# Kernel tuning notes

Hardware: AMD Instinct MI355X
Metric: run time of the kernel (lower is better)

## Reference

```python
import jax, jax.numpy as jnp
import numpy as np

N_NODES, N_EDGES, D_IN, D_HID, D_OUT = 50000, 800000, 128, 64, 32


def _glorot(key, shape):
    lim = jnp.sqrt(6.0 / (shape[0] + shape[1]))
    return jax.random.uniform(key, shape, minval=-lim, maxval=lim, dtype=jnp.float32)


def setup_inputs() -> dict:
    key = jax.random.key(0)
    ks = jax.random.split(key, 12)
    return {
        "x": jax.random.normal(ks[0], (N_NODES, D_IN), jnp.float32),
        "edge_index": jax.random.randint(ks[1], (2, N_EDGES), 0, N_NODES, dtype=jnp.int64),
        "edge_weight": jax.random.uniform(ks[2], (N_EDGES,), jnp.float32),
        # layer 1: GATv2Conv(D_IN -> D_HID, heads=1, edge_dim=1)
        "Wl1": _glorot(ks[3], (D_HID, D_IN)), "bl1": jnp.zeros((D_HID,), jnp.float32),
        "Wr1": _glorot(ks[4], (D_HID, D_IN)), "br1": jnp.zeros((D_HID,), jnp.float32),
        "We1": _glorot(ks[5], (D_HID, 1)),
        "att1": _glorot(ks[6], (1, D_HID))[0],
        "bias1": jnp.zeros((D_HID,), jnp.float32),
        # layer 2: GATv2Conv(D_HID -> D_OUT, heads=1, edge_dim=1)
        "Wl2": _glorot(ks[7], (D_OUT, D_HID)), "bl2": jnp.zeros((D_OUT,), jnp.float32),
        "Wr2": _glorot(ks[8], (D_OUT, D_HID)), "br2": jnp.zeros((D_OUT,), jnp.float32),
        "We2": _glorot(ks[9], (D_OUT, 1)),
        "att2": _glorot(ks[10], (1, D_OUT))[0],
        "bias2": jnp.zeros((D_OUT,), jnp.float32),
    }


def _segment_softmax(scores, seg, n):
    m = jax.ops.segment_max(scores, seg, num_segments=n)
    e = jnp.exp(scores - m[seg])
    s = jax.ops.segment_sum(e, seg, num_segments=n)
    return e / s[seg]


def _gatv2(x, src, dst, attr, Wl, bl, Wr, br, We, att, bias, n):
    # PyG GATv2Conv, heads=1, share_weights=False
    xl = x @ Wl.T + bl                    # source transform  [N, D]
    xr = x @ Wr.T + br                    # target transform  [N, D]
    ea = attr @ We.T                      # edge-attr embed   [E, D]
    m = jax.nn.leaky_relu(xl[src] + xr[dst] + ea, negative_slope=0.2)
    score = m @ att                       # [E]
    alpha = _segment_softmax(score, dst, n)
    out = jax.ops.segment_sum(alpha[:, None] * xl[src], dst, num_segments=n)
    return out + bias


def _forward(x, edge_index, edge_weight,
             Wl1, bl1, Wr1, br1, We1, att1, bias1,
             Wl2, bl2, Wr2, br2, We2, att2, bias2):
    n = x.shape[0]
    src, dst = edge_index[0], edge_index[1]
    attr = edge_weight[:, None]           # edge_dim = 1
    # PyG add_self_loops (default True) with fill_value='mean':
    # self-loop attr = mean of incoming edge_attr per node (0 if none)
    cnt = jax.ops.segment_sum(jnp.ones_like(edge_weight), dst, num_segments=n)
    loop_attr = jax.ops.segment_sum(attr, dst, num_segments=n) / jnp.maximum(cnt, 1.0)[:, None]
    loop = jnp.arange(n, dtype=src.dtype)
    src2 = jnp.concatenate([src, loop])
    dst2 = jnp.concatenate([dst, loop])
    attr2 = jnp.concatenate([attr, loop_attr], axis=0)
    h = jax.nn.elu(_gatv2(x, src2, dst2, attr2, Wl1, bl1, Wr1, br1, We1, att1, bias1, n))
    z = _gatv2(h, src2, dst2, attr2, Wl2, bl2, Wr2, br2, We2, att2, bias2, n)
    return jax.nn.softplus(z) + 0.0001


def reference(x, edge_index, edge_weight,
              Wl1, bl1, Wr1, br1, We1, att1, bias1,
              Wl2, bl2, Wr2, br2, We2, att2, bias2):
    return _forward(x, edge_index, edge_weight,
                    Wl1, bl1, Wr1, br1, We1, att1, bias1,
                    Wl2, bl2, Wr2, br2, We2, att2, bias2)
```

## Files before the change

kernel.cpp:

```cpp
#include <hip/hip_runtime.h>
#include <math.h>

typedef unsigned short ushort_t;
typedef __attribute__((ext_vector_type(8))) short bf16x8;
typedef __attribute__((ext_vector_type(4))) float f32x4;

#define NBLK  128
#define MAXNH 25024

template<int CTRL>
__device__ __forceinline__ float dpp_addf(float x)
{
    int y = __builtin_amdgcn_update_dpp(0, __float_as_int(x), CTRL, 0xf, 0xf, true);
    return x + __int_as_float(y);
}

template<int LPE>
__device__ __forceinline__ float group_reduce(float p)
{
    p = dpp_addf<0xB1>(p);
    p = dpp_addf<0x4E>(p);
    if constexpr (LPE >= 8)  p = dpp_addf<0x141>(p);
    if constexpr (LPE >= 16) p = dpp_addf<0x140>(p);
    return p;
}

__device__ __forceinline__ ushort_t f2bf(float f)
{
    unsigned u = __float_as_uint(f);
    return (ushort_t)((u + 0x7fffu + ((u >> 16) & 1u)) >> 16);
}

__global__ __launch_bounds__(256)
void setup_kernel(const float* __restrict__ Wl1, const float* __restrict__ Wr1,
                  const float* __restrict__ Wl2, const float* __restrict__ Wr2,
                  ushort_t* __restrict__ wab1, ushort_t* __restrict__ wab2)
{
    const int T = gridDim.x * 256;
    const int i0 = blockIdx.x * 256 + threadIdx.x;
    for (int k = i0; k < 2 * 64 * 128; k += T)
        wab1[k] = f2bf(k < 64 * 128 ? Wl1[k] : Wr1[k - 64 * 128]);
    for (int k = i0; k < 2 * 32 * 64; k += T)
        wab2[k] = f2bf(k < 32 * 64 ? Wl2[k] : Wr2[k - 32 * 64]);
}

__global__ __launch_bounds__(256, 1)
void count_hist(const int* __restrict__ ei, ushort_t* __restrict__ lrank,
                ushort_t* __restrict__ histG, int E, int n, int EPB)
{
    __shared__ unsigned h[MAXNH];
    const int tid = threadIdx.x;
    const int b   = blockIdx.x;
    const int nh  = (n + 1) >> 1;
    for (int i = tid; i < nh; i += 256) h[i] = 0u;
    __syncthreads();

    const int e0 = b * EPB;
    const int e1 = min(e0 + EPB, E);
    for (int e = e0 + tid; e < e1; e += 256) {
        int d = ei[E + e];
        unsigned sh  = (unsigned)(d & 1) * 16u;
        unsigned old = atomicAdd(&h[d >> 1], 1u << sh);
        lrank[e] = (ushort_t)((old >> sh) & 0xffffu);
    }
    __syncthreads();

    ushort_t* row = histG + (size_t)b * n;
    for (int i = tid; i < n; i += 256) {
        unsigned v = h[i >> 1];
        row[i] = (ushort_t)((v >> ((i & 1) * 16)) & 0xffffu);
    }
}

__global__ __launch_bounds__(256)
void col_scan(ushort_t* __restrict__ histG, int* __restrict__ cnt, int n)
{
    int idx = blockIdx.x * 256 + threadIdx.x;
    if (idx >= n) return;
    unsigned acc = 0;
    #pragma unroll 1
    for (int b0 = 0; b0 < NBLK; b0 += 16) {
        ushort_t c[16];
        #pragma unroll
        for (int j = 0; j < 16; ++j)
            c[j] = histG[(size_t)(b0 + j) * n + idx];
        #pragma unroll
        for (int j = 0; j < 16; ++j) {
            unsigned cc = c[j];
            histG[(size_t)(b0 + j) * n + idx] = (ushort_t)acc;
            acc += cc;
        }
    }
    cnt[idx] = (int)acc;
}

__global__ __launch_bounds__(256)
void scan_p1(const int* __restrict__ cnt, int* __restrict__ bsums, int n)
{
    __shared__ int s[256];
    const int tid = threadIdx.x;
    int gi = blockIdx.x * 256 + tid;
    s[tid] = (gi < n) ? cnt[gi] : 0;
    __syncthreads();
    #pragma unroll
    for (int off = 128; off >= 1; off >>= 1) {
        if (tid < off) s[tid] += s[tid + off];
        __syncthreads();
    }
    if (tid == 0) bsums[blockIdx.x] = s[0];
}

__global__ __launch_bounds__(256)
void scan_p3(const int* __restrict__ cnt, const int* __restrict__ bsums,
             int* __restrict__ row_off, int n, int nb)
{
    __shared__ int sb[256];
    __shared__ int s[256];
    const int tid = threadIdx.x;

    int bv = (tid < nb) ? bsums[tid] : 0;
    sb[tid] = bv;
    __syncthreads();
    #pragma unroll
    for (int off = 1; off < 256; off <<= 1) {
        int t = (tid >= off) ? sb[tid - off] : 0;
        __syncthreads();
        sb[tid] += t;
        __syncthreads();
    }
    int excl_t = sb[tid] - bv;
    __syncthreads();
    sb[tid] = excl_t;
    __syncthreads();
    const int base = sb[blockIdx.x];

    int gi = blockIdx.x * 256 + tid;
    int c = (gi < n) ? cnt[gi] : 0;
    s[tid] = c;
    __syncthreads();
    #pragma unroll
    for (int off = 1; off < 256; off <<= 1) {
        int t = (tid >= off) ? s[tid - off] : 0;
        __syncthreads();
        s[tid] += t;
        __syncthreads();
    }
    if (gi < n) {
        int excl = base + s[tid] - c;
        row_off[gi] = excl;
        if (gi == n - 1) row_off[n] = excl + c;
    }
}

template<int N, int K>
__global__ __launch_bounds__(256, 2)
void scat_plus_gemm(const int* __restrict__ ei, const float* __restrict__ ew,
                    const int* __restrict__ row_off,
                    const ushort_t* __restrict__ lrank,
                    const ushort_t* __restrict__ boff,
                    int2* __restrict__ slot,
                    int E, int n, int EPB, int scatBlocks,
                    const float* __restrict__ X, const ushort_t* __restrict__ Wab,
                    const float* __restrict__ ba, const float* __restrict__ bb,
                    ushort_t* __restrict__ OutA, ushort_t* __restrict__ OutB, int M)
{
    constexpr int KC = K / 32;
    constexpr int NT = N / 16;
    __shared__ ushort_t sW[N * K];
    __shared__ ushort_t sX[64 * K];
    const int tid = threadIdx.x;

    if (blockIdx.x < scatBlocks) {
        const int base = blockIdx.x * (256 * 8);
        #pragma unroll
        for (int k = 0; k < 8; ++k) {
            int e = base + k * 256 + tid;
            if (e < E) {
                int d  = ei[E + e];
                int hb = e / EPB;
                int pos = row_off[d] + (int)boff[(size_t)hb * n + d]
                                     + (int)lrank[e];
                slot[pos] = make_int2(ei[e], __float_as_int(ew[e]));
            }
        }
        return;
    }

    const int m0 = (blockIdx.x - scatBlocks) * 64;

    auto swz = [](int r, int e) {
        return r * K + ((((e >> 3) ^ (r & 7)) << 3) | (e & 7));
    };

    constexpr int WQ8 = N * K / 8;
    for (int q = tid; q < WQ8; q += 256) {
        int nrow = q / (K / 8);
        int e8   = (q % (K / 8)) * 8;
        uint4 v = *(const uint4*)(Wab + (size_t)nrow * K + e8);
        *(uint4*)&sW[swz(nrow, e8)] = v;
    }
    constexpr int XQ = 64 * (K / 4);
    for (int q = tid; q < XQ; q += 256) {
        int r  = q / (K / 4);
        int k4 = (q % (K / 4)) * 4;
        float4 v = make_float4(0.f, 0.f, 0.f, 0.f);
        int gr = m0 + r;
        if (gr < M) v = *(const float4*)(X + (size_t)gr * K + k4);
        short4 h = make_short4((short)f2bf(v.x), (short)f2bf(v.y),
                               (short)f2bf(v.z), (short)f2bf(v.w));
        *(short4*)&sX[swz(r, k4)] = h;
    }
    __syncthreads();

    const int wv   = tid >> 6;
    const int lane = tid & 63;
    const int mrow = lane & 15;
    const int quad = lane >> 4;

    bf16x8 a[KC];
    #pragma unroll
    for (int kc = 0; kc < KC; ++kc)
        a[kc] = *(const bf16x8*)&sX[swz(wv * 16 + mrow, kc * 32 + quad * 8)];

    #pragma unroll
    for (int nt = 0; nt < NT; ++nt) {
        f32x4 acc = {0.f, 0.f, 0.f, 0.f};
        #pragma unroll
        for (int kc = 0; kc < KC; ++kc) {
            bf16x8 bfr = *(const bf16x8*)&sW[swz(nt * 16 + mrow, kc * 32 + quad * 8)];
            acc = __builtin_amdgcn_mfma_f32_16x16x32_bf16(a[kc], bfr, acc, 0, 0, 0);
        }
        const int col = nt * 16 + mrow;
        ushort_t* dst;
        int cc;
        float bv;
        if (col < N / 2) { dst = OutA; cc = col;         bv = ba[cc]; }
        else             { dst = OutB; cc = col - N / 2; bv = bb[cc]; }
        #pragma unroll
        for (int r = 0; r < 4; ++r) {
            int row = m0 + wv * 16 + quad * 4 + r;
            if (row < M)
                dst[(size_t)row * (N / 2) + cc] = f2bf(acc[r] + bv);
        }
    }
}

template<int N, int K>
__global__ __launch_bounds__(256, 2)
void gemm_xw_mfma(const float* __restrict__ X, const ushort_t* __restrict__ Wab,
                  const float* __restrict__ ba, const float* __restrict__ bb,
                  ushort_t* __restrict__ OutA, ushort_t* __restrict__ OutB, int M)
{
    constexpr int KC = K / 32;
    constexpr int NT = N / 16;
    __shared__ ushort_t sW[N * K];
    __shared__ ushort_t sX[64 * K];
    const int tid = threadIdx.x;
    const int m0  = blockIdx.x * 64;

    auto swz = [](int r, int e) {
        return r * K + ((((e >> 3) ^ (r & 7)) << 3) | (e & 7));
    };

    constexpr int WQ8 = N * K / 8;
    for (int q = tid; q < WQ8; q += 256) {
        int nrow = q / (K / 8);
        int e8   = (q % (K / 8)) * 8;
        uint4 v = *(const uint4*)(Wab + (size_t)nrow * K + e8);
        *(uint4*)&sW[swz(nrow, e8)] = v;
    }
    constexpr int XQ = 64 * (K / 4);
    for (int q = tid; q < XQ; q += 256) {
        int r  = q / (K / 4);
        int k4 = (q % (K / 4)) * 4;
        float4 v = make_float4(0.f, 0.f, 0.f, 0.f);
        int gr = m0 + r;
        if (gr < M) v = *(const float4*)(X + (size_t)gr * K + k4);
        short4 h = make_short4((short)f2bf(v.x), (short)f2bf(v.y),
                               (short)f2bf(v.z), (short)f2bf(v.w));
        *(short4*)&sX[swz(r, k4)] = h;
    }
    __syncthreads();

    const int wv   = tid >> 6;
    const int lane = tid & 63;
    const int mrow = lane & 15;
    const int quad = lane >> 4;

    bf16x8 a[KC];
    #pragma unroll
    for (int kc = 0; kc < KC; ++kc)
        a[kc] = *(const bf16x8*)&sX[swz(wv * 16 + mrow, kc * 32 + quad * 8)];

    #pragma unroll
    for (int nt = 0; nt < NT; ++nt) {
        f32x4 acc = {0.f, 0.f, 0.f, 0.f};
        #pragma unroll
        for (int kc = 0; kc < KC; ++kc) {
            bf16x8 bfr = *(const bf16x8*)&sW[swz(nt * 16 + mrow, kc * 32 + quad * 8)];
            acc = __builtin_amdgcn_mfma_f32_16x16x32_bf16(a[kc], bfr, acc, 0, 0, 0);
        }
        const int col = nt * 16 + mrow;
        ushort_t* dst;
        int cc;
        float bv;
        if (col < N / 2) { dst = OutA; cc = col;         bv = ba[cc]; }
        else             { dst = OutB; cc = col - N / 2; bv = bb[cc]; }
        #pragma unroll
        for (int r = 0; r < 4; ++r) {
            int row = m0 + wv * 16 + quad * 4 + r;
            if (row < M)
                dst[(size_t)row * (N / 2) + cc] = f2bf(acc[r] + bv);
        }
    }
}

template<int D, int ACT>
__global__ __launch_bounds__(256)
void edge_attn(const ushort_t* __restrict__ xl, const ushort_t* __restrict__ xr,
               const float* __restrict__ We, const float* __restrict__ att,
               const float* __restrict__ bias,
               const int* __restrict__ row_off, const int2* __restrict__ slot,
               float* __restrict__ out, int n)
{
    constexpr int LPE = D / 4;
    constexpr int SG  = 64 / LPE;
    const int lane = threadIdx.x & 63;
    const int wid  = threadIdx.x >> 6;
    const int t    = lane % LPE;
    const int g    = lane / LPE;
    const int node = blockIdx.x * 4 + wid;
    if (node >= n) return;

    auto unpack = [](uint2 d) -> float4 {
        float4 r;
        r.x = __uint_as_float(d.x << 16);
        r.y = __uint_as_float(d.x & 0xffff0000u);
        r.z = __uint_as_float(d.y << 16);
        r.w = __uint_as_float(d.y & 0xffff0000u);
        return r;
    };

    const float4 We4   = *(const float4*)(We   + 4 * t);
    const float4 att4  = *(const float4*)(att  + 4 * t);
    const float4 bias4 = *(const float4*)(bias + 4 * t);
    const float4 xr4   = unpack(*(const uint2*)(xr + (size_t)node * D + 4 * t));

    const int start = row_off[node];
    const int end   = row_off[node + 1];
    const int R  = (end - start) / SG;
    const int jt = start + R * SG;
    const bool has_tail = jt < end;

    int2  q[4];
    uint2 xv[4];
    #pragma unroll
    for (int s = 0; s < 4; ++s) {
        if (s < R) {
            q[s]  = slot[start + s * SG + g];
            xv[s] = *(const uint2*)(xl + (size_t)q[s].x * D + 4 * t);
        }
    }
    int2 tq = make_int2(0, 0);
    uint2 tx = make_uint2(0u, 0u);
    if (has_tail) {
        int idx = min(jt + g, end - 1);
        tq = slot[idx];
        tx = *(const uint2*)(xl + (size_t)tq.x * D + 4 * t);
    }
    const uint2 xs = *(const uint2*)(xl + (size_t)node * D + 4 * t);

    float denom = 0.f, wsum = 0.f;
    float4 acc = make_float4(0.f, 0.f, 0.f, 0.f);

    auto body = [&](int2 qe, float4 xvv, bool active) {
        float w = __int_as_float(qe.y);
        float4 v;
        v.x = xvv.x + fmaf(w, We4.x, xr4.x);
        v.y = xvv.y + fmaf(w, We4.y, xr4.y);
        v.z = xvv.z + fmaf(w, We4.z, xr4.z);
        v.w = xvv.w + fmaf(w, We4.w, xr4.w);
        float4 m;
        m.x = fmaxf(v.x, 0.2f * v.x);
        m.y = fmaxf(v.y, 0.2f * v.y);
        m.z = fmaxf(v.z, 0.2f * v.z);
        m.w = fmaxf(v.w, 0.2f * v.w);
        float p = att4.x * m.x + att4.y * m.y + att4.z * m.z + att4.w * m.w;
        p = group_reduce<LPE>(p);
        float e = active ? __expf(p) : 0.f;
        wsum  += active ? w : 0.f;
        denom += e;
        acc.x = fmaf(e, xvv.x, acc.x);
        acc.y = fmaf(e, xvv.y, acc.y);
        acc.z = fmaf(e, xvv.z, acc.z);
        acc.w = fmaf(e, xvv.w, acc.w);
    };

    int b = 0;
    for (; b + 4 <= R; b += 4) {
        #pragma unroll
        for (int s = 0; s < 4; ++s) {
            int2 cq = q[s]; uint2 cx = xv[s];
            int nr = b + 4 + s;
            if (nr < R) {
                q[s]  = slot[start + nr * SG + g];
                xv[s] = *(const uint2*)(xl + (size_t)q[s].x * D + 4 * t);
            }
            body(cq, unpack(cx), true);
        }
    }
    #pragma unroll
    for (int s = 0; s < 4; ++s)
        if (b + s < R) body(q[s], unpack(xv[s]), true);

    if (has_tail)
        body(tq, unpack(tx), (jt + g) < end);

    #pragma unroll
    for (int mask = LPE; mask < 64; mask <<= 1) {
        denom += __shfl_xor(denom, mask);
        wsum  += __shfl_xor(wsum,  mask);
        acc.x += __shfl_xor(acc.x, mask);
        acc.y += __shfl_xor(acc.y, mask);
        acc.z += __shfl_xor(acc.z, mask);
        acc.w += __shfl_xor(acc.w, mask);
    }

    {
        float w = wsum / (float)max(end - start, 1);
        float4 xvs = unpack(xs);
        float4 v;
        v.x = xvs.x + fmaf(w, We4.x, xr4.x);
        v.y = xvs.y + fmaf(w, We4.y, xr4.y);
        v.z = xvs.z + fmaf(w, We4.z, xr4.z);
        v.w = xvs.w + fmaf(w, We4.w, xr4.w);
        float4 m;
        m.x = fmaxf(v.x, 0.2f * v.x);
        m.y = fmaxf(v.y, 0.2f * v.y);
        m.z = fmaxf(v.z, 0.2f * v.z);
        m.w = fmaxf(v.w, 0.2f * v.w);
        float p = att4.x * m.x + att4.y * m.y + att4.z * m.z + att4.w * m.w;
        p = group_reduce<LPE>(p);
        float e = __expf(p);
        denom += e;
        acc.x = fmaf(e, xvs.x, acc.x);
        acc.y = fmaf(e, xvs.y, acc.y);
        acc.z = fmaf(e, xvs.z, acc.z);
        acc.w = fmaf(e, xvs.w, acc.w);
    }

    float4 res;
    res.x = acc.x / denom + bias4.x;
    res.y = acc.y / denom + bias4.y;
    res.z = acc.z / denom + bias4.z;
    res.w = acc.w / denom + bias4.w;
    if (ACT == 0) {
        res.x = fmaxf(res.x, 0.f) + __expf(fminf(res.x, 0.f)) - 1.f;
        res.y = fmaxf(res.y, 0.f) + __expf(fminf(res.y, 0.f)) - 1.f;
        res.z = fmaxf(res.z, 0.f) + __expf(fminf(res.z, 0.f)) - 1.f;
        res.w = fmaxf(res.w, 0.f) + __expf(fminf(res.w, 0.f)) - 1.f;
    } else {
        res.x = fmaxf(res.x, 0.f) + __logf(1.f + __expf(-fabsf(res.x))) + 1e-4f;
        res.y = fmaxf(res.y, 0.f) + __logf(1.f + __expf(-fabsf(res.y))) + 1e-4f;
        res.z = fmaxf(res.z, 0.f) + __logf(1.f + __expf(-fabsf(res.z))) + 1e-4f;
        res.w = fmaxf(res.w, 0.f) + __logf(1.f + __expf(-fabsf(res.w))) + 1e-4f;
    }
    if (g == 0)
        *(float4*)(out + (size_t)node * D + 4 * t) = res;
}

extern "C" void kernel_launch(void* const* d_in, const int* in_sizes, int n_in,
                              void* d_out, int out_size, void* d_ws, size_t ws_size,
                              hipStream_t stream)
{
    const float* x     = (const float*)d_in[0];
    const int*   ei    = (const int*)d_in[1];
    const float* ew    = (const float*)d_in[2];
    const float* Wl1   = (const float*)d_in[3];
    const float* bl1   = (const float*)d_in[4];
    const float* Wr1   = (const float*)d_in[5];
    const float* br1   = (const float*)d_in[6];
    const float* We1   = (const float*)d_in[7];
    const float* att1  = (const float*)d_in[8];
    const float* bias1 = (const float*)d_in[9];
    const float* Wl2   = (const float*)d_in[10];
    const float* bl2   = (const float*)d_in[11];
    const float* Wr2   = (const float*)d_in[12];
    const float* br2   = (const float*)d_in[13];
    const float* We2   = (const float*)d_in[14];
    const float* att2  = (const float*)d_in[15];
    const float* bias2 = (const float*)d_in[16];
    float* out = (float*)d_out;

    const int n = in_sizes[0] / 128;
    const int E = in_sizes[2];
    const int NB = (n + 255) / 256;
    const int EPB = (E + NBLK - 1) / NBLK;
    const int scatBlocks = (E + 2047) / 2048;
    const int gemmBlocks = (n + 63) / 64;

    char* wp = (char*)d_ws;
    auto carve = [&](size_t bytes) -> void* {
        void* p = (void*)wp;
        wp += (bytes + 255) & ~(size_t)255;
        return p;
    };
    int*      cnt     = (int*)     carve((size_t)n * 4);
    int*      row_off = (int*)     carve((size_t)(n + 1) * 4);
    ushort_t* lrank   = (ushort_t*)carve((size_t)E * 2);
    ushort_t* histG   = (ushort_t*)carve((size_t)NBLK * n * 2);
    int*      bsums   = (int*)     carve((size_t)256 * 4);
    int2*     slot    = (int2*)    carve((size_t)E * 8);
    ushort_t* wab1    = (ushort_t*)carve((size_t)2 * 64 * 128 * 2);
    ushort_t* wab2    = (ushort_t*)carve((size_t)2 * 32 * 64 * 2);
    ushort_t* xl1     = (ushort_t*)carve((size_t)n * 64 * 2);
    ushort_t* xr1     = (ushort_t*)carve((size_t)n * 64 * 2);
    float*    hbuf    = (float*)   carve((size_t)n * 64 * 4);
    ushort_t* xl2     = (ushort_t*)carve((size_t)n * 32 * 2);
    ushort_t* xr2     = (ushort_t*)carve((size_t)n * 32 * 2);

    setup_kernel<<<256, 256, 0, stream>>>(Wl1, Wr1, Wl2, Wr2, wab1, wab2);

    count_hist<<<NBLK, 256, 0, stream>>>(ei, lrank, histG, E, n, EPB);
    col_scan  <<<NB, 256, 0, stream>>>(histG, cnt, n);
    scan_p1   <<<NB, 256, 0, stream>>>(cnt, bsums, n);
    scan_p3   <<<NB, 256, 0, stream>>>(cnt, bsums, row_off, n, NB);

    scat_plus_gemm<128, 128><<<scatBlocks + gemmBlocks, 256, 0, stream>>>(
        ei, ew, row_off, lrank, histG, slot, E, n, EPB, scatBlocks,
        x, wab1, bl1, br1, xl1, xr1, n);

    edge_attn<64, 0><<<(n + 3) / 4, 256, 0, stream>>>(xl1, xr1, We1, att1, bias1,
                                                      row_off, slot, hbuf, n);
    gemm_xw_mfma<64, 64><<<(n + 63) / 64, 256, 0, stream>>>(hbuf, wab2, bl2, br2,
                                                            xl2, xr2, n);
    edge_attn<32, 1><<<(n + 3) / 4, 256, 0, stream>>>(xl2, xr2, We2, att2, bias2,
                                                      row_off, slot, out, n);
}
```

Before: 244.0 us.

## Fold setup into histogram, fuse column scan with GEMM, scatter via LDS offsets

Weight bf16 conversion moves into an extra block of the histogram kernel. The column scan and block-sum reduction now run in the same launch as the layer-1 GEMM. The edge scatter becomes its own kernel with one block per histogram chunk, loading that block's offset row into LDS so the random global reads of per-block offsets disappear. This cuts the launch count and overlaps the scan with the GEMM, but the scatter now runs with only 128 blocks instead of being spread across the GEMM launch.

```diff
diff --git a/kernel.cpp b/kernel.cpp
--- a/kernel.cpp
+++ b/kernel.cpp
@@ -31,27 +31,27 @@
     return (ushort_t)((u + 0x7fffu + ((u >> 16) & 1u)) >> 16);
 }
 
-__global__ __launch_bounds__(256)
-void setup_kernel(const float* __restrict__ Wl1, const float* __restrict__ Wr1,
-                  const float* __restrict__ Wl2, const float* __restrict__ Wr2,
-                  ushort_t* __restrict__ wab1, ushort_t* __restrict__ wab2)
-{
-    const int T = gridDim.x * 256;
-    const int i0 = blockIdx.x * 256 + threadIdx.x;
-    for (int k = i0; k < 2 * 64 * 128; k += T)
-        wab1[k] = f2bf(k < 64 * 128 ? Wl1[k] : Wr1[k - 64 * 128]);
-    for (int k = i0; k < 2 * 32 * 64; k += T)
-        wab2[k] = f2bf(k < 32 * 64 ? Wl2[k] : Wr2[k - 32 * 64]);
-}
-
 __global__ __launch_bounds__(256, 1)
 void count_hist(const int* __restrict__ ei, ushort_t* __restrict__ lrank,
-                ushort_t* __restrict__ histG, int E, int n, int EPB)
-{
-    __shared__ unsigned h[MAXNH];
+                ushort_t* __restrict__ histG,
+                const float* __restrict__ Wl1, const float* __restrict__ Wr1,
+                const float* __restrict__ Wl2, const float* __restrict__ Wr2,
+                ushort_t* __restrict__ wab1, ushort_t* __restrict__ wab2,
+                int E, int n, int EPB)
+{
     const int tid = threadIdx.x;
     const int b   = blockIdx.x;
-    const int nh  = (n + 1) >> 1;
+
+    if (b == NBLK) {
+        for (int k = tid; k < 2 * 64 * 128; k += 256)
+            wab1[k] = f2bf(k < 64 * 128 ? Wl1[k] : Wr1[k - 64 * 128]);
+        for (int k = tid; k < 2 * 32 * 64; k += 256)
+            wab2[k] = f2bf(k < 32 * 64 ? Wl2[k] : Wr2[k - 32 * 64]);
+        return;
+    }
+
+    __shared__ unsigned h[MAXNH];
+    const int nh = (n + 1) >> 1;
     for (int i = tid; i < nh; i += 256) h[i] = 0u;
     __syncthreads();
 
@@ -72,121 +72,53 @@
     }
 }
 
-__global__ __launch_bounds__(256)
-void col_scan(ushort_t* __restrict__ histG, int* __restrict__ cnt, int n)
-{
-    int idx = blockIdx.x * 256 + threadIdx.x;
-    if (idx >= n) return;
-    unsigned acc = 0;
-    #pragma unroll 1
-    for (int b0 = 0; b0 < NBLK; b0 += 16) {
-        ushort_t c[16];
-        #pragma unroll
-        for (int j = 0; j < 16; ++j)
-            c[j] = histG[(size_t)(b0 + j) * n + idx];
-        #pragma unroll
-        for (int j = 0; j < 16; ++j) {
-            unsigned cc = c[j];
-            histG[(size_t)(b0 + j) * n + idx] = (ushort_t)acc;
-            acc += cc;
-        }
-    }
-    cnt[idx] = (int)acc;
-}
-
-__global__ __launch_bounds__(256)
-void scan_p1(const int* __restrict__ cnt, int* __restrict__ bsums, int n)
-{
-    __shared__ int s[256];
-    const int tid = threadIdx.x;
-    int gi = blockIdx.x * 256 + tid;
-    s[tid] = (gi < n) ? cnt[gi] : 0;
-    __syncthreads();
-    #pragma unroll
-    for (int off = 128; off >= 1; off >>= 1) {
-        if (tid < off) s[tid] += s[tid + off];
-        __syncthreads();
-    }
-    if (tid == 0) bsums[blockIdx.x] = s[0];
-}
-
-__global__ __launch_bounds__(256)
-void scan_p3(const int* __restrict__ cnt, const int* __restrict__ bsums,
-             int* __restrict__ row_off, int n, int nb)
-{
-    __shared__ int sb[256];
-    __shared__ int s[256];
-    const int tid = threadIdx.x;
-
-    int bv = (tid < nb) ? bsums[tid] : 0;
-    sb[tid] = bv;
-    __syncthreads();
-    #pragma unroll
-    for (int off = 1; off < 256; off <<= 1) {
-        int t = (tid >= off) ? sb[tid - off] : 0;
-        __syncthreads();
-        sb[tid] += t;
-        __syncthreads();
-    }
-    int excl_t = sb[tid] - bv;
-    __syncthreads();
-    sb[tid] = excl_t;
-    __syncthreads();
-    const int base = sb[blockIdx.x];
-
-    int gi = blockIdx.x * 256 + tid;
-    int c = (gi < n) ? cnt[gi] : 0;
-    s[tid] = c;
-    __syncthreads();
-    #pragma unroll
-    for (int off = 1; off < 256; off <<= 1) {
-        int t = (tid >= off) ? s[tid - off] : 0;
-        __syncthreads();
-        s[tid] += t;
-        __syncthreads();
-    }
-    if (gi < n) {
-        int excl = base + s[tid] - c;
-        row_off[gi] = excl;
-        if (gi == n - 1) row_off[n] = excl + c;
-    }
-}
-
 template<int N, int K>
 __global__ __launch_bounds__(256, 2)
-void scat_plus_gemm(const int* __restrict__ ei, const float* __restrict__ ew,
-                    const int* __restrict__ row_off,
-                    const ushort_t* __restrict__ lrank,
-                    const ushort_t* __restrict__ boff,
-                    int2* __restrict__ slot,
-                    int E, int n, int EPB, int scatBlocks,
-                    const float* __restrict__ X, const ushort_t* __restrict__ Wab,
-                    const float* __restrict__ ba, const float* __restrict__ bb,
-                    ushort_t* __restrict__ OutA, ushort_t* __restrict__ OutB, int M)
+void colscan_plus_gemm(ushort_t* __restrict__ histG, int* __restrict__ cnt,
+                       int* __restrict__ bsums, int n, int csBlocks,
+                       const float* __restrict__ X, const ushort_t* __restrict__ Wab,
+                       const float* __restrict__ ba, const float* __restrict__ bb,
+                       ushort_t* __restrict__ OutA, ushort_t* __restrict__ OutB,
+                       int M)
 {
     constexpr int KC = K / 32;
     constexpr int NT = N / 16;
     __shared__ ushort_t sW[N * K];
     __shared__ ushort_t sX[64 * K];
+    __shared__ int s[256];
     const int tid = threadIdx.x;
 
-    if (blockIdx.x < scatBlocks) {
-        const int base = blockIdx.x * (256 * 8);
-        #pragma unroll
-        for (int k = 0; k < 8; ++k) {
-            int e = base + k * 256 + tid;
-            if (e < E) {
-                int d  = ei[E + e];
-                int hb = e / EPB;
-                int pos = row_off[d] + (int)boff[(size_t)hb * n + d]
-                                     + (int)lrank[e];
-                slot[pos] = make_int2(ei[e], __float_as_int(ew[e]));
+    if (blockIdx.x < csBlocks) {
+        int idx = blockIdx.x * 256 + tid;
+        unsigned acc = 0;
+        if (idx < n) {
+            #pragma unroll 1
+            for (int b0 = 0; b0 < NBLK; b0 += 16) {
+                ushort_t c[16];
+                #pragma unroll
+                for (int j = 0; j < 16; ++j)
+                    c[j] = histG[(size_t)(b0 + j) * n + idx];
+                #pragma unroll
+                for (int j = 0; j < 16; ++j) {
+                    unsigned cc = c[j];
+                    histG[(size_t)(b0 + j) * n + idx] = (ushort_t)acc;
+                    acc += cc;
+                }
             }
-        }
+            cnt[idx] = (int)acc;
+        }
+        s[tid] = (idx < n) ? (int)acc : 0;
+        __syncthreads();
+        #pragma unroll
+        for (int off = 128; off >= 1; off >>= 1) {
+            if (tid < off) s[tid] += s[tid + off];
+            __syncthreads();
+        }
+        if (tid == 0) bsums[blockIdx.x] = s[0];
         return;
     }
 
-    const int m0 = (blockIdx.x - scatBlocks) * 64;
+    const int m0 = (blockIdx.x - csBlocks) * 64;
 
     auto swz = [](int r, int e) {
         return r * K + ((((e >> 3) ^ (r & 7)) << 3) | (e & 7));
@@ -241,6 +173,97 @@
             int row = m0 + wv * 16 + quad * 4 + r;
             if (row < M)
                 dst[(size_t)row * (N / 2) + cc] = f2bf(acc[r] + bv);
+        }
+    }
+}
+
+__global__ __launch_bounds__(256)
+void scan_p3(const int* __restrict__ cnt, const int* __restrict__ bsums,
+             int* __restrict__ row_off, int n, int nb)
+{
+    __shared__ int sb[256];
+    __shared__ int s[256];
+    const int tid = threadIdx.x;
+
+    int bv = (tid < nb) ? bsums[tid] : 0;
+    sb[tid] = bv;
+    __syncthreads();
+    #pragma unroll
+    for (int off = 1; off < 256; off <<= 1) {
+        int t = (tid >= off) ? sb[tid - off] : 0;
+        __syncthreads();
+        sb[tid] += t;
+        __syncthreads();
+    }
+    int excl_t = sb[tid] - bv;
+    __syncthreads();
+    sb[tid] = excl_t;
+    __syncthreads();
+    const int base = sb[blockIdx.x];
+
+    int gi = blockIdx.x * 256 + tid;
+    int c = (gi < n) ? cnt[gi] : 0;
+    s[tid] = c;
+    __syncthreads();
+    #pragma unroll
+    for (int off = 1; off < 256; off <<= 1) {
+        int t = (tid >= off) ? s[tid - off] : 0;
+        __syncthreads();
+        s[tid] += t;
+        __syncthreads();
+    }
+    if (gi < n) {
+        int excl = base + s[tid] - c;
+        row_off[gi] = excl;
+        if (gi == n - 1) row_off[n] = excl + c;
+    }
+}
+
+__global__ __launch_bounds__(256, 1)
+void scat_lds(const int* __restrict__ ei, const float* __restrict__ ew,
+              const int* __restrict__ row_off, const ushort_t* __restrict__ lrank,
+              const ushort_t* __restrict__ boff, int2* __restrict__ slot,
+              int E, int n, int EPB)
+{
+    __shared__ ushort_t sb[2 * MAXNH];
+    const int tid = threadIdx.x;
+    const int b   = blockIdx.x;
+
+    const ushort_t* row = boff + (size_t)b * n;
+    {
+        if ((n & 1) == 0 && (((size_t)b * n) & 1) == 0) {
+            const unsigned* r32 = (const unsigned*)row;
+            unsigned* s32 = (unsigned*)sb;
+            for (int i = tid; i < (n >> 1); i += 256) s32[i] = r32[i];
+        } else {
+            for (int i = tid; i < n; i += 256) sb[i] = row[i];
+        }
+    }
+    __syncthreads();
+
+    const int e0 = b * EPB;
+    const int e1 = min(e0 + EPB, E);
+    for (int base = e0 + tid; base < e1; base += 256 * 4) {
+        int dd[4], ss[4];
+        ushort_t rr[4];
+        float ww[4];
+        #pragma unroll
+        for (int j = 0; j < 4; ++j) {
+            int e = base + j * 256;
+            if (e < e1) {
+                dd[j] = ei[E + e];
+                rr[j] = lrank[e];
+                ss[j] = ei[e];
+                ww[j] = ew[e];
+            }
+        }
+        #pragma unroll
+        for (int j = 0; j < 4; ++j) {
+            int e = base + j * 256;
+            if (e < e1) {
+                int pos = row_off[dd[j]] + (int)sb[dd[j]] + (int)rr[j];
+                slot[pos] = make_int2(ss[j], __float_as_int(ww[j]));
+            }
         }
     }
 }
@@ -496,7 +519,6 @@
     const int E = in_sizes[2];
     const int NB = (n + 255) / 256;
     const int EPB = (E + NBLK - 1) / NBLK;
-    const int scatBlocks = (E + 2047) / 2048;
     const int gemmBlocks = (n + 63) / 64;
 
     char* wp = (char*)d_ws;
@@ -519,16 +541,14 @@
     ushort_t* xl2     = (ushort_t*)carve((size_t)n * 32 * 2);
     ushort_t* xr2     = (ushort_t*)carve((size_t)n * 32 * 2);
 
-    setup_kernel<<<256, 256, 0, stream>>>(Wl1, Wr1, Wl2, Wr2, wab1, wab2);
-
-    count_hist<<<NBLK, 256, 0, stream>>>(ei, lrank, histG, E, n, EPB);
-    col_scan  <<<NB, 256, 0, stream>>>(histG, cnt, n);
-    scan_p1   <<<NB, 256, 0, stream>>>(cnt, bsums, n);
-    scan_p3   <<<NB, 256, 0, stream>>>(cnt, bsums, row_off, n, NB);
-
-    scat_plus_gemm<128, 128><<<scatBlocks + gemmBlocks, 256, 0, stream>>>(
-        ei, ew, row_off, lrank, histG, slot, E, n, EPB, scatBlocks,
-        x, wab1, bl1, br1, xl1, xr1, n);
+    count_hist<<<NBLK + 1, 256, 0, stream>>>(ei, lrank, histG,
+                                             Wl1, Wr1, Wl2, Wr2, wab1, wab2,
+                                             E, n, EPB);
+    colscan_plus_gemm<128, 128><<<NB + gemmBlocks, 256, 0, stream>>>(
+        histG, cnt, bsums, n, NB, x, wab1, bl1, br1, xl1, xr1, n);
+    scan_p3<<<NB, 256, 0, stream>>>(cnt, bsums, row_off, n, NB);
+    scat_lds<<<NBLK, 256, 0, stream>>>(ei, ew, row_off, lrank, histG, slot,
+                                       E, n, EPB);
 
     edge_attn<64, 0><<<(n + 3) / 4, 256, 0, stream>>>(xl1, xr1, We1, att1, bias1,
                                                       row_off, slot, hbuf, n);
```

Result: no change. 241.9 us (-0.8%).
